# Kernel optimization log

Hardware: AMD Instinct MI355X
Metric: run time of the kernel (lower is better)

## Reference

```python
import jax, jax.numpy as jnp
import numpy as np
import math

NHEAD = 8
NEG = -1e9  # stand-in for float('-inf') in the torch mask

def _layernorm(x, g, b):
    m = x.mean(-1, keepdims=True)
    v = ((x - m) ** 2).mean(-1, keepdims=True)
    return (x - m) / jnp.sqrt(v + 1e-5) * g + b

def setup_inputs() -> dict:
    key = jax.random.key(0)
    ks = jax.random.split(key, 8)
    B, S, D, E, F, L, C = 32, 512, 9, 256, 1024, 4, 10
    p = lambda k, shape: jax.random.normal(k, shape, dtype=jnp.float32) * 0.02
    return dict(
        src=jax.random.normal(ks[0], (B, S, D), dtype=jnp.float32),
        emb_W=p(ks[1], (E, D)), emb_b=jnp.zeros((E,), jnp.float32),
        Wqkv=p(ks[2], (L, 3 * E, E)), bqkv=jnp.zeros((L, 3 * E), jnp.float32),
        Wo=p(ks[3], (L, E, E)), bo=jnp.zeros((L, E), jnp.float32),
        ln1_g=jnp.ones((L, E), jnp.float32), ln1_b=jnp.zeros((L, E), jnp.float32),
        ln2_g=jnp.ones((L, E), jnp.float32), ln2_b=jnp.zeros((L, E), jnp.float32),
        W1=p(ks[4], (L, F, E)), b1=jnp.zeros((L, F), jnp.float32),
        W2=p(ks[5], (L, E, F)), b2=jnp.zeros((L, E), jnp.float32),
        dec_W=p(ks[6], (C, E)),
    )

def reference(src, emb_W, emb_b, Wqkv, bqkv, Wo, bo, ln1_g, ln1_b,
              ln2_g, ln2_b, W1, b1, W2, b2, dec_W):
    B, S, _ = src.shape
    E = emb_W.shape[0]
    H = NHEAD
    hd = E // H
    L = Wqkv.shape[0]

    # custom sparse mask: diagonal-only attention, except the last query row
    # attends to everything but itself (has_src_mask=True branch)
    eye = jnp.eye(S, dtype=src.dtype)
    mask = jnp.where(eye > 0, 0.0, NEG)
    mask = mask.at[-1, :].set(0.0).at[-1, -1].set(NEG)

    # sinusoidal positional encoding [S, E]
    pos = jnp.arange(S, dtype=jnp.float32)[:, None]
    div = jnp.exp(jnp.arange(0, E, 2, dtype=jnp.float32) * (-math.log(10000.0) / E))
    pe = jnp.zeros((S, E), jnp.float32)
    pe = pe.at[:, 0::2].set(jnp.sin(pos * div)).at[:, 1::2].set(jnp.cos(pos * div))

    # embed + scale + pos-enc (batch-first layout; math identical to seq-first)
    x = (src @ emb_W.T + emb_b) * math.sqrt(E) + pe[None, :, :]

    attns = []
    for l in range(L):  # small fixed number of layers
        qkv = x @ Wqkv[l].T + bqkv[l]  # [B,S,3E]
        q, k, v = jnp.split(qkv, 3, axis=-1)
        rs = lambda t: t.reshape(B, S, H, hd).transpose(0, 2, 1, 3)  # [B,H,S,hd]
        q, k, v = rs(q), rs(k), rs(v)
        scores = jnp.einsum('bhqd,bhkd->bhqk', q, k) / math.sqrt(hd) + mask
        a = jax.nn.softmax(scores, axis=-1)
        attns.append(a.mean(axis=1))  # head-averaged attention, as torch MHA returns
        o = jnp.einsum('bhqk,bhkd->bhqd', a, v).transpose(0, 2, 1, 3).reshape(B, S, E)
        x = _layernorm(x + (o @ Wo[l].T + bo[l]), ln1_g[l], ln1_b[l])
        f = jax.nn.relu(x @ W1[l].T + b1[l]) @ W2[l].T + b2[l]
        x = _layernorm(x + f, ln2_g[l], ln2_b[l])

    x = jax.nn.relu(x)
    out = (x @ dec_W.T).mean(axis=1)  # mean over sequence
    out = jax.nn.log_softmax(out, axis=-1)
    return out, jnp.stack(attns)
```

## Files before the change

kernel.cpp:

```cpp
#include <hip/hip_runtime.h>
#include <hip/hip_bf16.h>
#include <math.h>

namespace {

constexpr int BATCH = 32;
constexpr int SEQ   = 512;
constexpr int DIN   = 9;
constexpr int EMB   = 256;
constexpr int FF    = 1024;
constexpr int NLAYER= 4;
constexpr int NCLS  = 10;
constexpr int NHEADS= 8;
constexpr int HDIM  = 32;
constexpr int NTOK  = BATCH*SEQ;

typedef __attribute__((ext_vector_type(8))) short short8;
typedef __attribute__((ext_vector_type(4))) float floatx4;

#define GLOAD_LDS16(g, l) __builtin_amdgcn_global_load_lds( \
    (const __attribute__((address_space(1))) unsigned*)(g), \
    (__attribute__((address_space(3))) unsigned*)(l), 16, 0, 0)

#define WAITCNT(N) asm volatile("s_waitcnt vmcnt(" #N ")" ::: "memory")

template<bool RELU, bool KV>
__global__ __launch_bounds__(256)
void gemm_mfma(const __hip_bfloat16* __restrict__ A, int lda,
               const __hip_bfloat16* __restrict__ W,
               const float* __restrict__ bias,
               __hip_bfloat16* __restrict__ C0,
               __hip_bfloat16* __restrict__ C1,
               int ldc, int K)
{
    __shared__ __hip_bfloat16 As[2*128*32];
    __shared__ __hip_bfloat16 Bs[2*128*32];
    const int bm = blockIdx.y*128, bn = blockIdx.x*128;
    const int tid  = threadIdx.x;
    const int lane = tid & 63;
    const int w    = tid >> 6;
    const int wm   = (w >> 1)*64, wn = (w & 1)*64;

    floatx4 acc[4][4] = {};

    const int srow = w*32 + (lane >> 2);
    const int scol = (lane & 3)*8;
    const __hip_bfloat16* gA0 = A + (size_t)(bm + srow)*lda + scol;
    const __hip_bfloat16* gA1 = A + (size_t)(bm + srow + 16)*lda + scol;
    const __hip_bfloat16* gB0 = W + (size_t)(bn + srow)*K + scol;
    const __hip_bfloat16* gB1 = W + (size_t)(bn + srow + 16)*K + scol;
    const int l0 = (w*2)*512, l1 = (w*2 + 1)*512;

#define GM_STAGE(buf, k0) do { \
    GLOAD_LDS16(gA0 + (k0), As + (buf)*4096 + l0); \
    GLOAD_LDS16(gA1 + (k0), As + (buf)*4096 + l1); \
    GLOAD_LDS16(gB0 + (k0), Bs + (buf)*4096 + l0); \
    GLOAD_LDS16(gB1 + (k0), Bs + (buf)*4096 + l1); } while (0)

    const int arow = wm + (lane & 15);
    const int brow = wn + (lane & 15);
    const int kh   = lane >> 4;
    const int nt   = K >> 5;

    GM_STAGE(0, 0);
    for (int t = 0; t < nt; t++) {
        const int cur = t & 1;
        if (t + 1 < nt) {
            GM_STAGE(cur ^ 1, (t+1)*32);
            WAITCNT(4);
        } else {
            WAITCNT(0);
        }
        __builtin_amdgcn_s_barrier();
        const short8* Ab = (const short8*)(As + cur*4096);
        const short8* Bb = (const short8*)(Bs + cur*4096);
        short8 af[4], bf[4];
        #pragma unroll
        for (int m = 0; m < 4; m++) af[m] = Ab[(arow + m*16)*4 + kh];
        #pragma unroll
        for (int n = 0; n < 4; n++) bf[n] = Bb[(brow + n*16)*4 + kh];
        #pragma unroll
        for (int m = 0; m < 4; m++)
            #pragma unroll
            for (int n = 0; n < 4; n++)
                acc[m][n] = __builtin_amdgcn_mfma_f32_16x16x32_bf16(af[m], bf[n], acc[m][n], 0, 0, 0);
        __builtin_amdgcn_s_barrier();
    }
#undef GM_STAGE

    __hip_bfloat16* Cb;
    int cb;
    if (KV && bn >= 256) { Cb = C1; cb = bn - 256; }
    else                 { Cb = C0; cb = bn; }

    const int crow0 = bm + wm + (lane >> 4)*4;
    #pragma unroll
    for (int n = 0; n < 4; n++) {
        const int coln = wn + (lane & 15) + n*16;
        const float bv = bias[bn + coln];
        #pragma unroll
        for (int m = 0; m < 4; m++) {
            #pragma unroll
            for (int r = 0; r < 4; r++) {
                int row = crow0 + m*16 + r;
                float v = acc[m][n][r] + bv;
                if (RELU) v = fmaxf(v, 0.f);
                Cb[(size_t)row*ldc + cb + coln] = __float2bfloat16(v);
            }
        }
    }
}

__device__ __forceinline__ void stageB(const __hip_bfloat16* __restrict__ W, int ldw,
                                       int rowbase, int kbase,
                                       __hip_bfloat16* LB, int buf, int w, int lane)
{
    #pragma unroll
    for (int i = 0; i < 4; i++) {
        int rc = 4*w + i;
        const __hip_bfloat16* src = W + (size_t)(rowbase + rc*16 + (lane >> 2))*ldw
                                      + kbase + (lane & 3)*8;
        GLOAD_LDS16(src, LB + buf*8192 + rc*512);
    }
}

__device__ __forceinline__ void mfma8(const short8* Ab, const short8* Bb,
                                      floatx4* acc, int rgrp, int colhalf,
                                      int cl, int kh)
{
    short8 af = Ab[rgrp*64 + cl*4 + kh];
    #pragma unroll
    for (int n = 0; n < 8; n++) {
        short8 bf = Bb[(colhalf*8 + n)*64 + cl*4 + kh];
        acc[n] = __builtin_amdgcn_mfma_f32_16x16x32_bf16(af, bf, acc[n], 0, 0, 0);
    }
}

__global__ __launch_bounds__(256, 2)
void layer_tail(const __hip_bfloat16* __restrict__ vbuf,
                const __hip_bfloat16* __restrict__ obuf,
                const __hip_bfloat16* __restrict__ Wo,
                const float* __restrict__ bo,
                const float* __restrict__ g1, const float* __restrict__ b1ln,
                const __hip_bfloat16* __restrict__ W1,
                const float* __restrict__ b1f,
                const __hip_bfloat16* __restrict__ W2,
                const float* __restrict__ b2f,
                const float* __restrict__ g2, const float* __restrict__ b2ln,
                __hip_bfloat16* __restrict__ xb16,
                const __hip_bfloat16* __restrict__ Wkv,
                const float* __restrict__ bk,
                const float* __restrict__ bv2,
                __hip_bfloat16* __restrict__ kout,
                __hip_bfloat16* __restrict__ vout)
{
    __shared__ __hip_bfloat16 SM[34816];
    __hip_bfloat16* LB = SM;
    __hip_bfloat16* LA = SM + 16384;
    __hip_bfloat16* X1 = SM + 18432;
    __hip_bfloat16* HC = SM + 26624;
    float* RED = (float*)LA;

    const int bm   = blockIdx.x*32;
    const int tid  = threadIdx.x;
    const int lane = tid & 63;
    const int w    = tid >> 6;
    const int rgrp = w & 1;
    const int colhalf = w >> 1;
    const int cl   = lane & 15;
    const int rg   = lane >> 4;
    const int kh   = lane >> 4;

    floatx4 acc[8] = {};
    const __hip_bfloat16* asrc = nullptr;
    if (w >= 2) {
        int a = w - 2;
        int grow = bm + a*16 + (lane >> 2);
        bool isl = (grow & (SEQ-1)) == (SEQ-1);
        asrc = (isl ? obuf + (size_t)(grow >> 9)*EMB
                    : vbuf + (size_t)grow*EMB) + (lane & 3)*8;
    }
    stageB(Wo, 256, 0, 0, LB, 0, w, lane);
    if (w >= 2) GLOAD_LDS16(asrc, LA + (w-2)*512);
    for (int t = 0; t < 8; t++) {
        const int cur = t & 1;
        if (t < 7) {
            stageB(Wo, 256, 0, (t+1)*32, LB, cur^1, w, lane);
            if (w >= 2) GLOAD_LDS16(asrc + (t+1)*32, LA + (cur^1)*1024 + (w-2)*512);
            WAITCNT(4);
        } else WAITCNT(0);
        __builtin_amdgcn_s_barrier();
        mfma8((const short8*)(LA + cur*1024), (const short8*)(LB + cur*8192),
              acc, rgrp, colhalf, cl, kh);
        __builtin_amdgcn_s_barrier();
    }
    {
        float gv[8], bbv[8], bv[8];
        #pragma unroll
        for (int n = 0; n < 8; n++) {
            int col = colhalf*128 + n*16 + cl;
            bv[n] = bo[col]; gv[n] = g1[col]; bbv[n] = b1ln[col];
        }
        #pragma unroll
        for (int r = 0; r < 4; r++) {
            int row = bm + rgrp*16 + rg*4 + r;
            const __hip_bfloat16* xr = xb16 + (size_t)row*EMB + colhalf*128;
            float S = 0.f, Q = 0.f;
            #pragma unroll
            for (int n = 0; n < 8; n++) {
                float v = acc[n][r] + bv[n] + __bfloat162float(xr[n*16 + cl]);
                acc[n][r] = v; S += v; Q += v*v;
            }
            #pragma unroll
            for (int o = 1; o < 16; o <<= 1) { S += __shfl_xor(S, o); Q += __shfl_xor(Q, o); }
            if (cl == 0) {
                int idx = rgrp*16 + rg*4 + r;
                RED[colhalf*32 + idx] = S;
                RED[64 + colhalf*32 + idx] = Q;
            }
        }
        __syncthreads();
        #pragma unroll
        for (int r = 0; r < 4; r++) {
            int idx = rgrp*16 + rg*4 + r;
            float S = RED[idx] + RED[32 + idx];
            float Q = RED[64 + idx] + RED[96 + idx];
            float mean = S * (1.f/EMB);
            float var  = Q * (1.f/EMB) - mean*mean;
            float rstd = 1.f / sqrtf(var + 1e-5f);
            #pragma unroll
            for (int n = 0; n < 8; n++) {
                int col = colhalf*128 + n*16 + cl;
                float v = (acc[n][r] - mean)*rstd*gv[n] + bbv[n];
                X1[(col >> 5)*1024 + rgrp*512 + (rg*4 + r)*32 + (col & 31)] = __float2bfloat16(v);
            }
        }
        __syncthreads();
    }

    floatx4 acc2[8] = {};
    for (int c = 0; c < 4; c++) {
        floatx4 fa[8] = {};
        stageB(W1, 256, c*256, 0, LB, 0, w, lane);
        for (int t = 0; t < 8; t++) {
            const int cur = t & 1;
            if (t < 7) { stageB(W1, 256, c*256, (t+1)*32, LB, cur^1, w, lane); WAITCNT(4); }
            else WAITCNT(0);
            __builtin_amdgcn_s_barrier();
            mfma8((const short8*)X1 + t*128, (const short8*)(LB + cur*8192),
                  fa, rgrp, colhalf, cl, kh);
            __builtin_amdgcn_s_barrier();
        }
        #pragma unroll
        for (int n = 0; n < 8; n++) {
            int colh = colhalf*128 + n*16 + cl;
            float bb = b1f[c*256 + colh];
            #pragma unroll
            for (int r = 0; r < 4; r++) {
                float v = fmaxf(fa[n][r] + bb, 0.f);
                HC[(colh >> 5)*1024 + rgrp*512 + (rg*4 + r)*32 + (colh & 31)] = __float2bfloat16(v);
            }
        }
        __syncthreads();
        stageB(W2, 1024, 0, c*256, LB, 0, w, lane);
        for (int t = 0; t < 8; t++) {
            const int cur = t & 1;
            if (t < 7) { stageB(W2, 1024, 0, c*256 + (t+1)*32, LB, cur^1, w, lane); WAITCNT(4); }
            else WAITCNT(0);
            __builtin_amdgcn_s_barrier();
            mfma8((const short8*)HC + t*128, (const short8*)(LB + cur*8192),
                  acc2, rgrp, colhalf, cl, kh);
            __builtin_amdgcn_s_barrier();
        }
    }

    {
        float gv[8], bbv[8], bv[8];
        #pragma unroll
        for (int n = 0; n < 8; n++) {
            int col = colhalf*128 + n*16 + cl;
            bv[n] = b2f[col]; gv[n] = g2[col]; bbv[n] = b2ln[col];
        }
        #pragma unroll
        for (int r = 0; r < 4; r++) {
            float S = 0.f, Q = 0.f;
            #pragma unroll
            for (int n = 0; n < 8; n++) {
                int col = colhalf*128 + n*16 + cl;
                float x1v = __bfloat162float(X1[(col >> 5)*1024 + rgrp*512 + (rg*4 + r)*32 + (col & 31)]);
                float v = acc2[n][r] + bv[n] + x1v;
                acc2[n][r] = v; S += v; Q += v*v;
            }
            #pragma unroll
            for (int o = 1; o < 16; o <<= 1) { S += __shfl_xor(S, o); Q += __shfl_xor(Q, o); }
            if (cl == 0) {
                int idx = rgrp*16 + rg*4 + r;
                RED[colhalf*32 + idx] = S;
                RED[64 + colhalf*32 + idx] = Q;
            }
        }
        __syncthreads();
        #pragma unroll
        for (int r = 0; r < 4; r++) {
            int idx = rgrp*16 + rg*4 + r;
            int row = bm + idx;
            float S = RED[idx] + RED[32 + idx];
            float Q = RED[64 + idx] + RED[96 + idx];
            float mean = S * (1.f/EMB);
            float var  = Q * (1.f/EMB) - mean*mean;
            float rstd = 1.f / sqrtf(var + 1e-5f);
            __hip_bfloat16* xr = xb16 + (size_t)row*EMB + colhalf*128;
            #pragma unroll
            for (int n = 0; n < 8; n++) {
                int col = colhalf*128 + n*16 + cl;
                float v = (acc2[n][r] - mean)*rstd*gv[n] + bbv[n];
                __hip_bfloat16 hv = __float2bfloat16(v);
                xr[n*16 + cl] = hv;
                HC[(col >> 5)*1024 + rgrp*512 + (rg*4 + r)*32 + (col & 31)] = hv;
            }
        }
    }

    if (Wkv != nullptr) {
        __syncthreads();
        #pragma unroll
        for (int nh = 0; nh < 2; nh++) {
            floatx4 a3[8] = {};
            const float* bkv = (nh == 0) ? bk : bv2;
            __hip_bfloat16* dst = (nh == 0) ? kout : vout;
            stageB(Wkv, 256, nh*256, 0, LB, 0, w, lane);
            for (int t = 0; t < 8; t++) {
                const int cur = t & 1;
                if (t < 7) { stageB(Wkv, 256, nh*256, (t+1)*32, LB, cur^1, w, lane); WAITCNT(4); }
                else WAITCNT(0);
                __builtin_amdgcn_s_barrier();
                mfma8((const short8*)HC + t*128, (const short8*)(LB + cur*8192),
                      a3, rgrp, colhalf, cl, kh);
                __builtin_amdgcn_s_barrier();
            }
            #pragma unroll
            for (int n = 0; n < 8; n++) {
                int col = colhalf*128 + n*16 + cl;
                float bb = bkv[col];
                #pragma unroll
                for (int r = 0; r < 4; r++) {
                    int row = bm + rgrp*16 + rg*4 + r;
                    dst[(size_t)row*EMB + col] = __float2bfloat16(a3[n][r] + bb);
                }
            }
        }
    }
}

__global__ void f2b_all(const float* __restrict__ s0, const float* __restrict__ s1,
                        const float* __restrict__ s2, const float* __restrict__ s3,
                        __hip_bfloat16* __restrict__ d0, __hip_bfloat16* __restrict__ d1,
                        __hip_bfloat16* __restrict__ d2, __hip_bfloat16* __restrict__ d3)
{
    int blk = blockIdx.x;
    const float* s; __hip_bfloat16* d; int base;
    if      (blk <  768) { s = s0; d = d0; base = blk; }
    else if (blk < 1024) { s = s1; d = d1; base = blk - 768; }
    else if (blk < 2048) { s = s2; d = d2; base = blk - 1024; }
    else                 { s = s3; d = d3; base = blk - 2048; }
    int i = (base*256 + threadIdx.x)*4;
    float4 v = *(const float4*)(s + i);
    __hip_bfloat16 tmp[4];
    tmp[0] = __float2bfloat16(v.x); tmp[1] = __float2bfloat16(v.y);
    tmp[2] = __float2bfloat16(v.z); tmp[3] = __float2bfloat16(v.w);
    *(ushort4*)(d + i) = *(const ushort4*)tmp;
}

__global__ void embed_kernel(const float* __restrict__ src,
                             const float* __restrict__ emb_W,
                             const float* __restrict__ emb_b,
                             __hip_bfloat16* __restrict__ xb)
{
    int row = blockIdx.x;
    int e = threadIdx.x;
    int s = row % SEQ;
    const float* sr = src + (size_t)row*DIN;
    float acc = emb_b[e];
    #pragma unroll
    for (int d = 0; d < DIN; d++) acc += sr[d]*emb_W[e*DIN + d];
    acc *= 16.0f;
    int i2 = e & ~1;
    float div = expf(-(float)i2 * (9.210340371976184f / (float)EMB));
    float ang = (float)s * div;
    float pe = (e & 1) ? cosf(ang) : sinf(ang);
    xb[(size_t)row*EMB + e] = __float2bfloat16(acc + pe);
}

__global__ __launch_bounds__(512)
void attn_last_head(const __hip_bfloat16* __restrict__ xb,
                    const __hip_bfloat16* __restrict__ Wq,
                    const float* __restrict__ bq,
                    const __hip_bfloat16* __restrict__ kbuf,
                    const __hip_bfloat16* __restrict__ vbuf,
                    __hip_bfloat16* __restrict__ obuf,
                    float* __restrict__ amh)
{
    const int h = blockIdx.x, b = blockIdx.y;
    const int t = threadIdx.x;
    __shared__ float xlast[EMB];
    __shared__ float qpart[HDIM][17];
    __shared__ float qh[HDIM];
    __shared__ float sc[SEQ];
    __shared__ float red1[8], red2[8];
    __shared__ float opart[16][HDIM];

    if (t < EMB) xlast[t] = __bfloat162float(xb[((size_t)b*SEQ + SEQ-1)*EMB + t]);
    __syncthreads();

    {
        int d = t & 31, c = t >> 5;
        const __hip_bfloat16* wr = Wq + (size_t)(h*HDIM + d)*EMB + c*16;
        short8 w0 = *(const short8*)(wr);
        short8 w1 = *(const short8*)(wr + 8);
        float p = 0.f;
        #pragma unroll
        for (int j = 0; j < 8; j++)
            p += xlast[c*16 + j]*__bfloat162float(((const __hip_bfloat16*)&w0)[j]);
        #pragma unroll
        for (int j = 0; j < 8; j++)
            p += xlast[c*16 + 8 + j]*__bfloat162float(((const __hip_bfloat16*)&w1)[j]);
        qpart[d][c] = p;
    }
    __syncthreads();
    if (t < HDIM) {
        float qv = bq[h*HDIM + t];
        #pragma unroll
        for (int c = 0; c < 16; c++) qv += qpart[t][c];
        qh[t] = qv;
    }
    __syncthreads();

    {
        const __hip_bfloat16* krow = kbuf + ((size_t)b*SEQ + t)*EMB + h*HDIM;
        float s = 0.f;
        #pragma unroll
        for (int vv = 0; vv < 4; vv++) {
            short8 kk = *(const short8*)(krow + vv*8);
            #pragma unroll
            for (int j = 0; j < 8; j++)
                s += qh[vv*8 + j]*__bfloat162float(((const __hip_bfloat16*)&kk)[j]);
        }
        s *= 0.17677669529663687f;
        if (t == SEQ-1) s += -1e9f;
        sc[t] = s;
    }
    __syncthreads();

    {
        int wv = t >> 6, lane = t & 63;
        float m = sc[t];
        #pragma unroll
        for (int o = 32; o; o >>= 1) m = fmaxf(m, __shfl_xor(m, o));
        if (lane == 0) red1[wv] = m;
        __syncthreads();
        m = red1[0];
        #pragma unroll
        for (int i = 1; i < 8; i++) m = fmaxf(m, red1[i]);
        float e = expf(sc[t] - m);
        float s = e;
        #pragma unroll
        for (int o = 32; o; o >>= 1) s += __shfl_xor(s, o);
        if (lane == 0) red2[wv] = s;
        __syncthreads();
        float tot = red2[0]+red2[1]+red2[2]+red2[3]+red2[4]+red2[5]+red2[6]+red2[7];
        float a = e / tot;
        sc[t] = a;
        amh[((size_t)b*NHEADS + h)*SEQ + t] = a;
    }
    __syncthreads();

    {
        int e = t & 31, part = t >> 5;
        float o = 0.f;
        const __hip_bfloat16* vc = vbuf + (size_t)b*SEQ*EMB + h*HDIM + e;
        for (int k = part*32; k < part*32 + 32; k++)
            o += sc[k]*__bfloat162float(vc[(size_t)k*EMB]);
        opart[part][e] = o;
    }
    __syncthreads();
    if (t < HDIM) {
        float o = 0.f;
        #pragma unroll
        for (int p = 0; p < 16; p++) o += opart[p][t];
        obuf[b*EMB + h*HDIM + t] = __float2bfloat16(o);
    }
}

__global__ void write_attns(float* __restrict__ attns, const float* __restrict__ amh_all)
{
    constexpr int PER_ROW = SEQ/4;
    size_t tid = (size_t)blockIdx.x*blockDim.x + threadIdx.x;
    size_t row = tid / PER_ROW;
    int c4 = (int)(tid % PER_ROW);
    int q = (int)(row % SEQ);
    float4 v = make_float4(0.f,0.f,0.f,0.f);
    if (q == SEQ-1) {
        size_t lb = row / SEQ;
        const float* base = amh_all + lb*NHEADS*SEQ + c4*4;
        float x0=0.f, x1=0.f, x2=0.f, x3=0.f;
        #pragma unroll
        for (int h = 0; h < NHEADS; h++) {
            const float* r = base + (size_t)h*SEQ;
            x0 += r[0]; x1 += r[1]; x2 += r[2]; x3 += r[3];
        }
        v = make_float4(x0*0.125f, x1*0.125f, x2*0.125f, x3*0.125f);
    } else if ((q >> 2) == c4) {
        ((float*)&v)[q & 3] = 1.f;
    }
    ((float4*)attns)[tid] = v;
}

__global__ __launch_bounds__(512)
void decode_fused(const __hip_bfloat16* __restrict__ xb, const float* __restrict__ dec_W,
                  float* __restrict__ out)
{
    int b = blockIdx.x, t = threadIdx.x;
    int e = t & 255, half = t >> 8;
    __shared__ float rs[2][256];
    {
        const __hip_bfloat16* xp = xb + ((size_t)b*SEQ + half*256)*EMB + e;
        float r = 0.f;
        for (int i = 0; i < 256; i++) r += fmaxf(__bfloat162float(xp[(size_t)i*EMB]), 0.f);
        rs[half][e] = r;
    }
    __syncthreads();
    float part[NCLS];
    if (t < 256) {
        float rr = rs[0][t] + rs[1][t];
        #pragma unroll
        for (int c = 0; c < NCLS; c++) part[c] = rr * dec_W[c*EMB + t];
    } else {
        #pragma unroll
        for (int c = 0; c < NCLS; c++) part[c] = 0.f;
    }
    #pragma unroll
    for (int o = 32; o; o >>= 1)
        #pragma unroll
        for (int c = 0; c < NCLS; c++) part[c] += __shfl_xor(part[c], o);
    __shared__ float red[8][NCLS];
    int wv = t >> 6, lane = t & 63;
    if (lane == 0)
        #pragma unroll
        for (int c = 0; c < NCLS; c++) red[wv][c] = part[c];
    __syncthreads();
    if (t == 0) {
        float lg[NCLS];
        float m = -1e30f;
        #pragma unroll
        for (int c = 0; c < NCLS; c++) {
            float s = 0.f;
            #pragma unroll
            for (int wvi = 0; wvi < 8; wvi++) s += red[wvi][c];
            lg[c] = s * (1.f/(float)SEQ);
            m = fmaxf(m, lg[c]);
        }
        float s = 0.f;
        #pragma unroll
        for (int c = 0; c < NCLS; c++) s += expf(lg[c] - m);
        float ls = logf(s);
        #pragma unroll
        for (int c = 0; c < NCLS; c++) out[b*NCLS + c] = lg[c] - m - ls;
    }
}

}

extern "C" void kernel_launch(void* const* d_in, const int* in_sizes, int n_in,
                              void* d_out, int out_size, void* d_ws, size_t ws_size,
                              hipStream_t stream)
{
    const float* src   = (const float*)d_in[0];
    const float* emb_W = (const float*)d_in[1];
    const float* emb_b = (const float*)d_in[2];
    const float* Wqkv  = (const float*)d_in[3];
    const float* bqkv  = (const float*)d_in[4];
    const float* Wo    = (const float*)d_in[5];
    const float* bo    = (const float*)d_in[6];
    const float* ln1_g = (const float*)d_in[7];
    const float* ln1_b = (const float*)d_in[8];
    const float* ln2_g = (const float*)d_in[9];
    const float* ln2_b = (const float*)d_in[10];
    const float* W1    = (const float*)d_in[11];
    const float* b1    = (const float*)d_in[12];
    const float* W2    = (const float*)d_in[13];
    const float* b2    = (const float*)d_in[14];
    const float* dec_W = (const float*)d_in[15];

    float* out   = (float*)d_out;
    float* attns = out + BATCH*NCLS;

    char* ws = (char*)d_ws;
    __hip_bfloat16* xb16 = (__hip_bfloat16*)ws;     ws += (size_t)NTOK*EMB*2;
    __hip_bfloat16* kbuf = (__hip_bfloat16*)ws;     ws += (size_t)NTOK*EMB*2;
    __hip_bfloat16* vbuf = (__hip_bfloat16*)ws;     ws += (size_t)NTOK*EMB*2;
    __hip_bfloat16* obuf = (__hip_bfloat16*)ws;     ws += (size_t)BATCH*EMB*2;
    __hip_bfloat16* wq16 = (__hip_bfloat16*)ws;     ws += (size_t)NLAYER*3*EMB*EMB*2;
    __hip_bfloat16* wo16 = (__hip_bfloat16*)ws;     ws += (size_t)NLAYER*EMB*EMB*2;
    __hip_bfloat16* w116 = (__hip_bfloat16*)ws;     ws += (size_t)NLAYER*FF*EMB*2;
    __hip_bfloat16* w216 = (__hip_bfloat16*)ws;     ws += (size_t)NLAYER*EMB*FF*2;
    float*          amall= (float*)ws;              ws += (size_t)NLAYER*BATCH*NHEADS*SEQ*4;

    f2b_all<<<3072, 256, 0, stream>>>(Wqkv, Wo, W1, W2, wq16, wo16, w116, w216);

    embed_kernel<<<NTOK, EMB, 0, stream>>>(src, emb_W, emb_b, xb16);

    gemm_mfma<false, true><<<dim3(512/128, NTOK/128), 256, 0, stream>>>(
        xb16, EMB, wq16 + (size_t)EMB*EMB, bqkv + EMB, kbuf, vbuf, EMB, EMB);

    for (int l = 0; l < NLAYER; l++) {
        const __hip_bfloat16* wql = wq16 + (size_t)l*3*EMB*EMB;
        const float* bql = bqkv + (size_t)l*3*EMB;

        attn_last_head<<<dim3(NHEADS, BATCH), 512, 0, stream>>>(
            xb16, wql, bql, kbuf, vbuf, obuf, amall + (size_t)l*BATCH*NHEADS*SEQ);

        const bool last = (l == NLAYER-1);
        const __hip_bfloat16* wkv_next = last ? nullptr
            : wq16 + (size_t)(l+1)*3*EMB*EMB + (size_t)EMB*EMB;
        const float* bk_next = last ? nullptr : bqkv + (size_t)(l+1)*3*EMB + EMB;
        const float* bv_next = last ? nullptr : bqkv + (size_t)(l+1)*3*EMB + 2*EMB;
        layer_tail<<<NTOK/32, 256, 0, stream>>>(
            vbuf, obuf,
            wo16 + (size_t)l*EMB*EMB, bo + (size_t)l*EMB,
            ln1_g + l*EMB, ln1_b + l*EMB,
            w116 + (size_t)l*FF*EMB, b1 + (size_t)l*FF,
            w216 + (size_t)l*EMB*FF, b2 + (size_t)l*EMB,
            ln2_g + l*EMB, ln2_b + l*EMB,
            xb16,
            wkv_next, bk_next, bv_next,
            last ? nullptr : kbuf, last ? nullptr : vbuf);
    }

    {
        size_t total_f4 = (size_t)NLAYER*BATCH*SEQ*(SEQ/4);
        int blocks = (int)((total_f4 + 255)/256);
        write_attns<<<blocks, 256, 0, stream>>>(attns, amall);
    }

    decode_fused<<<BATCH, 512, 0, stream>>>(xb16, dec_W, out);
}
```

Measured before the change: 481.4 us.

## Double layer_tail row tile to 64 with 512 threads and triple-buffered weight staging

The fused layer_tail kernel now processes 64 token rows per block with 8 waves instead of 32 rows with 4 waves. Each staged weight tile is therefore reused across twice as many rows, which halves global weight traffic per token. Weight and activation staging moves from double to triple buffering with a two-step prefetch distance, to hide load latency. The cost is much more LDS (about 124 KB per block) and higher register pressure, which may cut occupancy to one block per CU.

```diff
diff --git a/kernel.cpp b/kernel.cpp
--- a/kernel.cpp
+++ b/kernel.cpp
@@ -111,13 +111,13 @@
     }
 }
 
-__device__ __forceinline__ void stageB(const __hip_bfloat16* __restrict__ W, int ldw,
-                                       int rowbase, int kbase,
-                                       __hip_bfloat16* LB, int buf, int w, int lane)
+__device__ __forceinline__ void stageB64(const __hip_bfloat16* __restrict__ W, int ldw,
+                                         int rowbase, int kbase,
+                                         __hip_bfloat16* LB, int buf, int w, int lane)
 {
     #pragma unroll
-    for (int i = 0; i < 4; i++) {
-        int rc = 4*w + i;
+    for (int i = 0; i < 2; i++) {
+        int rc = 2*w + i;
         const __hip_bfloat16* src = W + (size_t)(rowbase + rc*16 + (lane >> 2))*ldw
                                       + kbase + (lane & 3)*8;
         GLOAD_LDS16(src, LB + buf*8192 + rc*512);
@@ -136,7 +136,7 @@
     }
 }
 
-__global__ __launch_bounds__(256, 2)
+__global__ __launch_bounds__(512, 2)
 void layer_tail(const __hip_bfloat16* __restrict__ vbuf,
                 const __hip_bfloat16* __restrict__ obuf,
                 const __hip_bfloat16* __restrict__ Wo,
@@ -154,43 +154,47 @@
                 __hip_bfloat16* __restrict__ kout,
                 __hip_bfloat16* __restrict__ vout)
 {
-    __shared__ __hip_bfloat16 SM[34816];
+    __shared__ __hip_bfloat16 SM[63488];
     __hip_bfloat16* LB = SM;
-    __hip_bfloat16* LA = SM + 16384;
-    __hip_bfloat16* X1 = SM + 18432;
-    __hip_bfloat16* HC = SM + 26624;
+    __hip_bfloat16* LA = SM + 24576;
+    __hip_bfloat16* X1 = SM + 30720;
+    __hip_bfloat16* HC = SM + 47104;
     float* RED = (float*)LA;
 
-    const int bm   = blockIdx.x*32;
+    const int bm   = blockIdx.x*64;
     const int tid  = threadIdx.x;
     const int lane = tid & 63;
     const int w    = tid >> 6;
-    const int rgrp = w & 1;
-    const int colhalf = w >> 1;
+    const int rgrp = w & 3;
+    const int colhalf = w >> 2;
     const int cl   = lane & 15;
     const int rg   = lane >> 4;
-    const int kh   = lane >> 4;
+    const int kh   = rg;
 
     floatx4 acc[8] = {};
     const __hip_bfloat16* asrc = nullptr;
-    if (w >= 2) {
-        int a = w - 2;
+    if (w >= 4) {
+        int a = w - 4;
         int grow = bm + a*16 + (lane >> 2);
         bool isl = (grow & (SEQ-1)) == (SEQ-1);
         asrc = (isl ? obuf + (size_t)(grow >> 9)*EMB
                     : vbuf + (size_t)grow*EMB) + (lane & 3)*8;
     }
-    stageB(Wo, 256, 0, 0, LB, 0, w, lane);
-    if (w >= 2) GLOAD_LDS16(asrc, LA + (w-2)*512);
+    stageB64(Wo, 256, 0, 0, LB, 0, w, lane);
+    if (w >= 4) GLOAD_LDS16(asrc, LA + (w-4)*512);
+    stageB64(Wo, 256, 0, 32, LB, 1, w, lane);
+    if (w >= 4) GLOAD_LDS16(asrc + 32, LA + 2048 + (w-4)*512);
     for (int t = 0; t < 8; t++) {
-        const int cur = t & 1;
-        if (t < 7) {
-            stageB(Wo, 256, 0, (t+1)*32, LB, cur^1, w, lane);
-            if (w >= 2) GLOAD_LDS16(asrc + (t+1)*32, LA + (cur^1)*1024 + (w-2)*512);
-            WAITCNT(4);
-        } else WAITCNT(0);
+        const int cur = t % 3;
+        if (t + 2 < 8) {
+            const int nb = (t+2) % 3;
+            stageB64(Wo, 256, 0, (t+2)*32, LB, nb, w, lane);
+            if (w >= 4) GLOAD_LDS16(asrc + (t+2)*32, LA + nb*2048 + (w-4)*512);
+        }
+        if (w >= 4) { if (t < 6) WAITCNT(6); else if (t == 6) WAITCNT(3); else WAITCNT(0); }
+        else        { if (t < 6) WAITCNT(4); else if (t == 6) WAITCNT(2); else WAITCNT(0); }
         __builtin_amdgcn_s_barrier();
-        mfma8((const short8*)(LA + cur*1024), (const short8*)(LB + cur*8192),
+        mfma8((const short8*)(LA + cur*2048), (const short8*)(LB + cur*8192),
               acc, rgrp, colhalf, cl, kh);
         __builtin_amdgcn_s_barrier();
     }
@@ -215,16 +219,16 @@
             for (int o = 1; o < 16; o <<= 1) { S += __shfl_xor(S, o); Q += __shfl_xor(Q, o); }
             if (cl == 0) {
                 int idx = rgrp*16 + rg*4 + r;
-                RED[colhalf*32 + idx] = S;
-                RED[64 + colhalf*32 + idx] = Q;
+                RED[colhalf*64 + idx] = S;
+                RED[128 + colhalf*64 + idx] = Q;
             }
         }
         __syncthreads();
         #pragma unroll
         for (int r = 0; r < 4; r++) {
             int idx = rgrp*16 + rg*4 + r;
-            float S = RED[idx] + RED[32 + idx];
-            float Q = RED[64 + idx] + RED[96 + idx];
+            float S = RED[idx] + RED[64 + idx];
+            float Q = RED[128 + idx] + RED[192 + idx];
             float mean = S * (1.f/EMB);
             float var  = Q * (1.f/EMB) - mean*mean;
             float rstd = 1.f / sqrtf(var + 1e-5f);
@@ -232,7 +236,7 @@
             for (int n = 0; n < 8; n++) {
                 int col = colhalf*128 + n*16 + cl;
                 float v = (acc[n][r] - mean)*rstd*gv[n] + bbv[n];
-                X1[(col >> 5)*1024 + rgrp*512 + (rg*4 + r)*32 + (col & 31)] = __float2bfloat16(v);
+                X1[(col >> 5)*2048 + rgrp*512 + (rg*4 + r)*32 + (col & 31)] = __float2bfloat16(v);
             }
         }
         __syncthreads();
@@ -241,13 +245,14 @@
     floatx4 acc2[8] = {};
     for (int c = 0; c < 4; c++) {
         floatx4 fa[8] = {};
-        stageB(W1, 256, c*256, 0, LB, 0, w, lane);
+        stageB64(W1, 256, c*256, 0, LB, 0, w, lane);
+        stageB64(W1, 256, c*256, 32, LB, 1, w, lane);
         for (int t = 0; t < 8; t++) {
-            const int cur = t & 1;
-            if (t < 7) { stageB(W1, 256, c*256, (t+1)*32, LB, cur^1, w, lane); WAITCNT(4); }
-            else WAITCNT(0);
+            const int cur = t % 3;
+            if (t + 2 < 8) stageB64(W1, 256, c*256, (t+2)*32, LB, (t+2)%3, w, lane);
+            if (t < 6) WAITCNT(4); else if (t == 6) WAITCNT(2); else WAITCNT(0);
             __builtin_amdgcn_s_barrier();
-            mfma8((const short8*)X1 + t*128, (const short8*)(LB + cur*8192),
+            mfma8((const short8*)X1 + t*256, (const short8*)(LB + cur*8192),
                   fa, rgrp, colhalf, cl, kh);
             __builtin_amdgcn_s_barrier();
         }
@@ -258,17 +263,18 @@
             #pragma unroll
             for (int r = 0; r < 4; r++) {
                 float v = fmaxf(fa[n][r] + bb, 0.f);
-                HC[(colh >> 5)*1024 + rgrp*512 + (rg*4 + r)*32 + (colh & 31)] = __float2bfloat16(v);
+                HC[(colh >> 5)*2048 + rgrp*512 + (rg*4 + r)*32 + (colh & 31)] = __float2bfloat16(v);
             }
         }
         __syncthreads();
-        stageB(W2, 1024, 0, c*256, LB, 0, w, lane);
+        stageB64(W2, 1024, 0, c*256, LB, 0, w, lane);
+        stageB64(W2, 1024, 0, c*256 + 32, LB, 1, w, lane);
         for (int t = 0; t < 8; t++) {
-            const int cur = t & 1;
-            if (t < 7) { stageB(W2, 1024, 0, c*256 + (t+1)*32, LB, cur^1, w, lane); WAITCNT(4); }
-            else WAITCNT(0);
+            const int cur = t % 3;
+            if (t + 2 < 8) stageB64(W2, 1024, 0, c*256 + (t+2)*32, LB, (t+2)%3, w, lane);
+            if (t < 6) WAITCNT(4); else if (t == 6) WAITCNT(2); else WAITCNT(0);
             __builtin_amdgcn_s_barrier();
-            mfma8((const short8*)HC + t*128, (const short8*)(LB + cur*8192),
+            mfma8((const short8*)HC + t*256, (const short8*)(LB + cur*8192),
                   acc2, rgrp, colhalf, cl, kh);
             __builtin_amdgcn_s_barrier();
         }
@@ -287,7 +293,7 @@
             #pragma unroll
             for (int n = 0; n < 8; n++) {
                 int col = colhalf*128 + n*16 + cl;
-                float x1v = __bfloat162float(X1[(col >> 5)*1024 + rgrp*512 + (rg*4 + r)*32 + (col & 31)]);
+                float x1v = __bfloat162float(X1[(col >> 5)*2048 + rgrp*512 + (rg*4 + r)*32 + (col & 31)]);
                 float v = acc2[n][r] + bv[n] + x1v;
                 acc2[n][r] = v; S += v; Q += v*v;
             }
@@ -295,8 +301,8 @@
             for (int o = 1; o < 16; o <<= 1) { S += __shfl_xor(S, o); Q += __shfl_xor(Q, o); }
             if (cl == 0) {
                 int idx = rgrp*16 + rg*4 + r;
-                RED[colhalf*32 + idx] = S;
-                RED[64 + colhalf*32 + idx] = Q;
+                RED[colhalf*64 + idx] = S;
+                RED[128 + colhalf*64 + idx] = Q;
             }
         }
         __syncthreads();
@@ -304,8 +310,8 @@
         for (int r = 0; r < 4; r++) {
             int idx = rgrp*16 + rg*4 + r;
             int row = bm + idx;
-            float S = RED[idx] + RED[32 + idx];
-            float Q = RED[64 + idx] + RED[96 + idx];
+            float S = RED[idx] + RED[64 + idx];
+            float Q = RED[128 + idx] + RED[192 + idx];
             float mean = S * (1.f/EMB);
             float var  = Q * (1.f/EMB) - mean*mean;
             float rstd = 1.f / sqrtf(var + 1e-5f);
@@ -316,25 +322,26 @@
                 float v = (acc2[n][r] - mean)*rstd*gv[n] + bbv[n];
                 __hip_bfloat16 hv = __float2bfloat16(v);
                 xr[n*16 + cl] = hv;
-                HC[(col >> 5)*1024 + rgrp*512 + (rg*4 + r)*32 + (col & 31)] = hv;
-            }
-        }
+                HC[(col >> 5)*2048 + rgrp*512 + (rg*4 + r)*32 + (col & 31)] = hv;
+            }
+        }
+        __syncthreads();
     }
 
     if (Wkv != nullptr) {
-        __syncthreads();
         #pragma unroll
         for (int nh = 0; nh < 2; nh++) {
             floatx4 a3[8] = {};
             const float* bkv = (nh == 0) ? bk : bv2;
             __hip_bfloat16* dst = (nh == 0) ? kout : vout;
-            stageB(Wkv, 256, nh*256, 0, LB, 0, w, lane);
+            stageB64(Wkv, 256, nh*256, 0, LB, 0, w, lane);
+            stageB64(Wkv, 256, nh*256, 32, LB, 1, w, lane);
             for (int t = 0; t < 8; t++) {
-                const int cur = t & 1;
-                if (t < 7) { stageB(Wkv, 256, nh*256, (t+1)*32, LB, cur^1, w, lane); WAITCNT(4); }
-                else WAITCNT(0);
+                const int cur = t % 3;
+                if (t + 2 < 8) stageB64(Wkv, 256, nh*256, (t+2)*32, LB, (t+2)%3, w, lane);
+                if (t < 6) WAITCNT(4); else if (t == 6) WAITCNT(2); else WAITCNT(0);
                 __builtin_amdgcn_s_barrier();
-                mfma8((const short8*)HC + t*128, (const short8*)(LB + cur*8192),
+                mfma8((const short8*)HC + t*256, (const short8*)(LB + cur*8192),
                       a3, rgrp, colhalf, cl, kh);
                 __builtin_amdgcn_s_barrier();
             }
@@ -624,7 +631,7 @@
             : wq16 + (size_t)(l+1)*3*EMB*EMB + (size_t)EMB*EMB;
         const float* bk_next = last ? nullptr : bqkv + (size_t)(l+1)*3*EMB + EMB;
         const float* bv_next = last ? nullptr : bqkv + (size_t)(l+1)*3*EMB + 2*EMB;
-        layer_tail<<<NTOK/32, 256, 0, stream>>>(
+        layer_tail<<<NTOK/64, 512, 0, stream>>>(
             vbuf, obuf,
             wo16 + (size_t)l*EMB*EMB, bo + (size_t)l*EMB,
             ln1_g + l*EMB, ln1_b + l*EMB,
```

Result: faster. 444.5 us (-7.7%).
